# Kernel optimization log

Hardware: AMD Instinct MI355X
Metric: run time of the kernel (lower is better)

## Reference

```python
import jax, jax.numpy as jnp
import numpy as np

B, N, L = 32, 256, 50
DU, DI, DC = 32, 32, 16          # user / item / cate embed dims
D = DI + DC                       # item_feat_size = 48
N_USERS, N_ITEMS, N_CATES = 10001, 100000, 1001


def _linear_init(key, fan_in, fan_out):
    k1, k2 = jax.random.split(key)
    lim = 1.0 / np.sqrt(fan_in)
    w = jax.random.uniform(k1, (fan_in, fan_out), jnp.float32, -lim, lim)
    b = jax.random.uniform(k2, (fan_out,), jnp.float32, -lim, lim)
    return w, b


def setup_inputs() -> dict:
    key = jax.random.key(0)
    ks = jax.random.split(key, 16)

    def emb(k, n, d):
        # xavier-ish init, padding row 0 zeroed (padding_idx=0)
        t = jax.random.normal(k, (n, d), jnp.float32) * 0.02
        return t.at[0].set(0.0)

    emb_user = emb(ks[0], N_USERS, DU)
    emb_item = emb(ks[1], N_ITEMS, DI)
    emb_cate = emb(ks[2], N_CATES, DC)

    att_w1, att_b1 = _linear_init(ks[3], 4 * D, 64)   # LAU fc1 layer 1
    att_w2, att_b2 = _linear_init(ks[4], 64, 16)      # LAU fc1 layer 2
    att_w3, att_b3 = _linear_init(ks[5], 16, 1)       # LAU fc2

    TOT = DU + 2 * DI + 2 * DC                        # 128
    fc_w1, fc_b1 = _linear_init(ks[6], TOT, 200)
    fc_w2, fc_b2 = _linear_init(ks[7], 200, 80)
    fc_w3, fc_b3 = _linear_init(ks[8], 80, 1)

    user = jax.random.randint(ks[9], (B, N), 0, N_USERS)
    items = jax.random.randint(ks[10], (B, N), 0, N_ITEMS)
    items_cate = jax.random.randint(ks[11], (B, N), 0, N_CATES)
    interest_items = jax.random.randint(ks[12], (B, N, L), 0, N_ITEMS)
    interest_items_cate = jax.random.randint(ks[13], (B, N, L), 0, N_CATES)

    return dict(emb_user=emb_user, emb_item=emb_item, emb_cate=emb_cate,
                att_w1=att_w1, att_b1=att_b1, att_w2=att_w2, att_b2=att_b2,
                att_w3=att_w3, att_b3=att_b3,
                fc_w1=fc_w1, fc_b1=fc_b1, fc_w2=fc_w2, fc_b2=fc_b2,
                fc_w3=fc_w3, fc_b3=fc_b3,
                user=user, items=items, items_cate=items_cate,
                interest_items=interest_items,
                interest_items_cate=interest_items_cate)


def reference(emb_user, emb_item, emb_cate,
              att_w1, att_b1, att_w2, att_b2, att_w3, att_b3,
              fc_w1, fc_b1, fc_w2, fc_b2, fc_w3, fc_b3,
              user, items, items_cate, interest_items, interest_items_cate):
    u = emb_user[user]                                                 # [B,N,DU]
    ie = jnp.concatenate([emb_item[items], emb_cate[items_cate]], -1)  # [B,N,D]
    he = jnp.concatenate([emb_item[interest_items],
                          emb_cate[interest_items_cate]], -1)          # [B,N,L,D]

    # DIN local activation unit: cat(q, k, q-k, q*k) -> MLP -> scalar score
    q = jnp.broadcast_to(ie[:, :, None, :], he.shape)                  # [B,N,L,D]
    ai = jnp.concatenate([q, he, q - he, q * he], -1)                  # [B,N,L,4D]
    h = jax.nn.relu(ai @ att_w1 + att_b1)                              # [B,N,L,64]
    h = h @ att_w2 + att_b2                                            # [B,N,L,16]
    score = (h @ att_w3 + att_b3)[..., 0]                              # [B,N,L]

    # masked_fill(mask, 0) where mask = (interest_items == 0)
    score = jnp.where(interest_items == 0, 0.0, score)
    pooled = jnp.einsum('bnl,bnld->bnd', score, he)                    # [B,N,D]

    feat = jnp.concatenate([ie, pooled, u], -1)                        # [B,N,128]
    x = jax.nn.relu(feat @ fc_w1 + fc_b1)
    x = jax.nn.relu(x @ fc_w2 + fc_b2)
    logits = jax.nn.sigmoid((x @ fc_w3 + fc_b3)[..., 0])               # [B,N]

    logits = jnp.where(items == 0, -jnp.inf, logits)
    return jax.nn.softmax(logits, axis=-1)
```

## Files before the change

kernel.cpp:

```cpp
#include <hip/hip_runtime.h>
#include <hip/hip_bf16.h>
#include <math.h>


typedef short short8 __attribute__((ext_vector_type(8)));
typedef float f32x4 __attribute__((ext_vector_type(4)));

#define NL 50
#define BN_TOT 8192

__device__ __forceinline__ ushort f2bf(float x) {
    union { __hip_bfloat16 b; ushort u; } c;
    c.b = __float2bfloat16(x);
    return c.u;
}
__device__ __forceinline__ float bf2f(ushort h) {
    union { uint u; float f; } v; v.u = ((uint)h) << 16;
    return v.f;
}
__device__ __forceinline__ void wave_lds_fence() {
    asm volatile("s_waitcnt lgkmcnt(0)" ::: "memory");
}

#define WS_FEAT   0
#define WS_LOGITS 2097152
#define WS_W1FRAG 2129920
#define WS_W2FRAG 2183168
#define WS_WCFRAG 2226176
#define WS_WACF   2238464
#define WS_W23    2250752
#define WS_C23    2251008

__global__ __launch_bounds__(256) void k0_prep(
    const float* __restrict__ aw1, const float* __restrict__ ab1,
    const float* __restrict__ ab2,
    const float* __restrict__ aw2, const float* __restrict__ aw3,
    const float* __restrict__ ab3,
    const float* __restrict__ fw1, const float* __restrict__ fw2,
    ushort* __restrict__ W1frag, ushort* __restrict__ W2frag,
    ushort* __restrict__ WcFrag, ushort* __restrict__ WacF,
    float* __restrict__ w23, float* __restrict__ c23)
{
    const int b = blockIdx.x, t = threadIdx.x;
    if (b < 104) {
        int e = b * 256 + t;
        if (e < 26624) {
            int f = e >> 9, r = e & 511, l = r >> 3, j = r & 7;
            int nt = f >> 2, ks = f & 3;
            int k = ks * 32 + (l >> 4) * 8 + j, n = nt * 16 + (l & 15);
            float v = (n < 200) ? fw1[k * 200 + n] : 0.f;
            W1frag[e] = f2bf(v);
        }
    } else if (b < 188) {
        int e = (b - 104) * 256 + t;
        if (e < 21504) {
            int f = e >> 9, r = e & 511, l = r >> 3, j = r & 7;
            int nt = f / 7, ks = f % 7;
            int k = ks * 32 + (l >> 4) * 8 + j, n = nt * 16 + (l & 15);
            float v = (k < 200 && n < 80) ? fw2[k * 80 + n] : 0.f;
            W2frag[e] = f2bf(v);
        }
    } else if (b < 212) {
        int e = (b - 188) * 256 + t;
        int f = e >> 9, r = e & 511, l = r >> 3, j = r & 7;
        int nt = f / 3, ks = f % 3;
        int k = ks * 32 + (l >> 4) * 8 + j, n = nt * 16 + (l & 15);
        float v = (k < 48) ? (aw1[(48 + k) * 64 + n] - aw1[(96 + k) * 64 + n])
                           : aw1[(144 + (k - 48)) * 64 + n];
        WcFrag[e] = f2bf(v);
    } else if (b < 228) {
        int e = (b - 212) * 256 + t;
        int f = e >> 9, r = e & 511, l = r >> 3, j = r & 7;
        int nt = f >> 1, ks = f & 1;
        int k = ks * 32 + (l >> 4) * 8 + j, n = nt * 16 + (l & 15);
        float v = (k < 48) ? (aw1[k * 64 + n] + aw1[(96 + k) * 64 + n])
                           : ((k == 48) ? ab1[n] : 0.f);
        WacF[e] = f2bf(v);
    } else {
        if (t < 64) {
            float s = 0.f;
            #pragma unroll
            for (int jj = 0; jj < 16; ++jj) s = fmaf(aw2[t * 16 + jj], aw3[jj], s);
            w23[t] = s;
        }
        if (t == 64) {
            float c = ab3[0];
            #pragma unroll
            for (int jj = 0; jj < 16; ++jj) c = fmaf(ab2[jj], aw3[jj], c);
            c23[0] = c;
        }
    }
}

__device__ __forceinline__ short8 lds8(const ushort* hb, int row, int c) {
    return *(const short8*)&hb[row * 56 + c * 8];
}
__device__ __forceinline__ short8 scale8(const ushort* hb, const float* qv,
                                         int row, int c, int qb) {
    short8 a = lds8(hb, row, c);
    union { short8 v; ushort s[8]; } o;
    const ushort* as = (const ushort*)&a;
    #pragma unroll
    for (int j = 0; j < 8; ++j) o.s[j] = f2bf(bf2f(as[j]) * qv[qb + j]);
    return o.v;
}

__global__ __launch_bounds__(256, 4) void kA_attn(
    const float* __restrict__ emb_user,
    const float* __restrict__ emb_item,
    const float* __restrict__ emb_cate,
    const int* __restrict__ user,
    const int* __restrict__ items,
    const int* __restrict__ cates,
    const int* __restrict__ ii,
    const int* __restrict__ ic,
    const ushort* __restrict__ WcFrag,
    const ushort* __restrict__ WacF,
    const float* __restrict__ w23g,
    const float* __restrict__ c23g,
    ushort* __restrict__ feat)
{
    __shared__ __align__(16) ushort heb[4][64 * 56];
    __shared__ __align__(16) float  qf[4][48];
    __shared__ __align__(16) float  uf[4][32];
    __shared__ __align__(16) float  qcl[4][64];
    __shared__ __align__(16) float  scl[4][52];
    __shared__ int    iml[4][52];
    __shared__ int    icl[4][52];

    const int t = threadIdx.x;
    const int w = t >> 6, l = t & 63;
    const int bn = blockIdx.x * 4 + w;
    const int col = l & 15, g = l >> 4;

    ushort* hb = &heb[w][0];
    const float* qv = &qf[w][0];

    if (l < 12) {
        int it_ = items[bn], ct = cates[bn];
        float4 v = (l < 8) ? ((const float4*)emb_item)[(size_t)it_ * 8 + l]
                           : ((const float4*)emb_cate)[(size_t)ct * 4 + (l - 8)];
        *(float4*)&qf[w][l * 4] = v;
    } else if (l >= 16 && l < 24) {
        int ur = user[bn];
        *(float4*)&uf[w][(l - 16) * 4] = ((const float4*)emb_user)[(size_t)ur * 8 + (l - 16)];
    }
    if (l < NL) {
        iml[w][l] = ii[(size_t)bn * NL + l];
        icl[w][l] = ic[(size_t)bn * NL + l];
    }
    wave_lds_fence();

    #pragma unroll
    for (int e0 = 0; e0 < 300; e0 += 64) {
        int e = e0 + l;
        if (e < 300) {
            int row = e / 6, c = e - row * 6;
            int k0 = c * 8;
            const float* src = (k0 < 32)
                ? emb_item + (size_t)iml[w][row] * 32 + k0
                : emb_cate + (size_t)icl[w][row] * 16 + (k0 - 32);
            float4 f0 = *(const float4*)src;
            float4 f1 = *(const float4*)(src + 4);
            union { short8 v; ushort s[8]; } o;
            o.s[0] = f2bf(f0.x); o.s[1] = f2bf(f0.y); o.s[2] = f2bf(f0.z); o.s[3] = f2bf(f0.w);
            o.s[4] = f2bf(f1.x); o.s[5] = f2bf(f1.y); o.s[6] = f2bf(f1.z); o.s[7] = f2bf(f1.w);
            *(short8*)&hb[row * 56 + c * 8] = o.v;
        }
    }
    wave_lds_fence();

    {
        short8 afq[2];
        #pragma unroll
        for (int ks = 0; ks < 2; ++ks) {
            union { short8 v; ushort s[8]; } a;
            a.v = short8{0,0,0,0,0,0,0,0};
            if (col == 0) {
                int k0 = ks * 32 + g * 8;
                if (k0 < 48) {
                    float4 x = *(const float4*)&qf[w][k0];
                    float4 y = *(const float4*)&qf[w][k0 + 4];
                    a.s[0] = f2bf(x.x); a.s[1] = f2bf(x.y); a.s[2] = f2bf(x.z); a.s[3] = f2bf(x.w);
                    a.s[4] = f2bf(y.x); a.s[5] = f2bf(y.y); a.s[6] = f2bf(y.z); a.s[7] = f2bf(y.w);
                } else if (k0 == 48) {
                    a.s[0] = 0x3F80;
                }
            }
            afq[ks] = a.v;
        }
        f32x4 aq[4];
        #pragma unroll
        for (int nt = 0; nt < 4; ++nt) {
            aq[nt] = f32x4{0,0,0,0};
            #pragma unroll
            for (int ks = 0; ks < 2; ++ks) {
                short8 bq = *(const short8*)&WacF[((nt * 2 + ks) * 64 + l) * 8];
                aq[nt] = __builtin_amdgcn_mfma_f32_16x16x32_bf16(afq[ks], bq, aq[nt], 0, 0, 0);
            }
        }
        if (g == 0) {
            #pragma unroll
            for (int nt = 0; nt < 4; ++nt) qcl[w][nt * 16 + col] = aq[nt][0];
        }
    }

    f32x4 acc[4][4];
    #pragma unroll
    for (int m = 0; m < 4; ++m)
        #pragma unroll
        for (int n = 0; n < 4; ++n) acc[m][n] = f32x4{0,0,0,0};

    #pragma unroll
    for (int ks = 0; ks < 3; ++ks) {
        short8 af[4];
        #pragma unroll
        for (int mt = 0; mt < 4; ++mt) {
            int row = mt * 16 + col;
            if (ks == 0)       af[mt] = lds8(hb, row, g);
            else if (ks == 1)  af[mt] = (g < 2) ? lds8(hb, row, 4 + g)
                                                : scale8(hb, qv, row, g - 2, (g - 2) * 8);
            else               af[mt] = scale8(hb, qv, row, 2 + g, 16 + g * 8);
        }
        #pragma unroll
        for (int nt = 0; nt < 4; ++nt) {
            short8 bf = *(const short8*)&WcFrag[((nt * 3 + ks) * 64 + l) * 8];
            #pragma unroll
            for (int mt = 0; mt < 4; ++mt)
                acc[mt][nt] = __builtin_amdgcn_mfma_f32_16x16x32_bf16(af[mt], bf, acc[mt][nt], 0, 0, 0);
        }
    }
    wave_lds_fence();

    {
        float qcv[4], wv[4];
        #pragma unroll
        for (int nt = 0; nt < 4; ++nt) {
            qcv[nt] = qcl[w][nt * 16 + col];
            wv[nt]  = w23g[nt * 16 + col];
        }
        float c23 = c23g[0];
        #pragma unroll
        for (int mt = 0; mt < 4; ++mt) {
            #pragma unroll
            for (int i = 0; i < 4; ++i) {
                float s = fmaxf(acc[mt][0][i] + qcv[0], 0.f) * wv[0]
                        + fmaxf(acc[mt][1][i] + qcv[1], 0.f) * wv[1]
                        + fmaxf(acc[mt][2][i] + qcv[2], 0.f) * wv[2]
                        + fmaxf(acc[mt][3][i] + qcv[3], 0.f) * wv[3];
                s += __shfl_xor(s, 1, 16);
                s += __shfl_xor(s, 2, 16);
                s += __shfl_xor(s, 4, 16);
                s += __shfl_xor(s, 8, 16);
                int row = mt * 16 + g * 4 + i;
                if (col == 0 && row < NL)
                    scl[w][row] = (iml[w][row] == 0) ? 0.f : (s + c23);
            }
        }
    }
    wave_lds_fence();

    const size_t fb = (size_t)bn * 128;
    if (l < 48) {
        float p = 0.f;
        #pragma unroll
        for (int r4 = 0; r4 < 48; r4 += 4) {
            float4 sv = *(const float4*)&scl[w][r4];
            p = fmaf(sv.x, bf2f(hb[(r4 + 0) * 56 + l]), p);
            p = fmaf(sv.y, bf2f(hb[(r4 + 1) * 56 + l]), p);
            p = fmaf(sv.z, bf2f(hb[(r4 + 2) * 56 + l]), p);
            p = fmaf(sv.w, bf2f(hb[(r4 + 3) * 56 + l]), p);
        }
        float2 st = *(const float2*)&scl[w][48];
        p = fmaf(st.x, bf2f(hb[48 * 56 + l]), p);
        p = fmaf(st.y, bf2f(hb[49 * 56 + l]), p);
        feat[fb + 48 + l] = f2bf(p);
        feat[fb + l] = f2bf(qv[l]);
    }
    if (l < 32) feat[fb + 96 + l] = f2bf(uf[w][l]);
}

__global__ __launch_bounds__(64, 4) void k2_fc(
    const ushort* __restrict__ feat,
    const ushort* __restrict__ W1frag,
    const ushort* __restrict__ W2frag,
    const float* __restrict__ fb1, const float* __restrict__ fb2,
    const float* __restrict__ fw3, const float* __restrict__ fb3,
    const int* __restrict__ items,
    float* __restrict__ logits)
{
    __shared__ __align__(16) ushort x1s[16 * 256];

    const int l = threadIdx.x;
    const int r0 = blockIdx.x * 16;
    const int col = l & 15, g = l >> 4;

    short8 afr[4];
    #pragma unroll
    for (int ks = 0; ks < 4; ++ks)
        afr[ks] = *(const short8*)&feat[(size_t)(r0 + col) * 128 + ks * 32 + g * 8];

    f32x4 acc[13];
    #pragma unroll
    for (int nt = 0; nt < 13; ++nt) acc[nt] = f32x4{0,0,0,0};
    #pragma unroll
    for (int nt = 0; nt < 13; ++nt)
        #pragma unroll
        for (int ks = 0; ks < 4; ++ks) {
            short8 bf = *(const short8*)&W1frag[((nt * 4 + ks) * 64 + l) * 8];
            acc[nt] = __builtin_amdgcn_mfma_f32_16x16x32_bf16(afr[ks], bf, acc[nt], 0, 0, 0);
        }

    if (l < 32) {
        int row = l >> 1, c = 26 + (l & 1);
        *(short8*)&x1s[row * 256 + ((c ^ (row & 7)) << 3)] = short8{0,0,0,0,0,0,0,0};
    }
    #pragma unroll
    for (int nt = 0; nt < 13; ++nt) {
        int n = nt * 16 + col;
        float bias = (n < 200) ? fb1[n] : 0.f;
        #pragma unroll
        for (int i = 0; i < 4; ++i) {
            int row = g * 4 + i;
            float v = fmaxf(acc[nt][i] + bias, 0.f);
            int sw = (n >> 3) ^ (row & 7);
            x1s[row * 256 + sw * 8 + (n & 7)] = f2bf(v);
        }
    }
    wave_lds_fence();

    f32x4 acc2[6];
    #pragma unroll
    for (int nt = 0; nt < 6; ++nt) acc2[nt] = f32x4{0,0,0,0};
    #pragma unroll
    for (int ks = 0; ks < 7; ++ks) {
        int chunk = ks * 4 + g;
        short8 a = *(const short8*)&x1s[col * 256 + ((chunk ^ (col & 7)) << 3)];
        #pragma unroll
        for (int nt = 0; nt < 6; ++nt) {
            short8 bf = *(const short8*)&W2frag[((nt * 7 + ks) * 64 + l) * 8];
            acc2[nt] = __builtin_amdgcn_mfma_f32_16x16x32_bf16(a, bf, acc2[nt], 0, 0, 0);
        }
    }

    {
        float s[4] = {0.f, 0.f, 0.f, 0.f};
        #pragma unroll
        for (int nt = 0; nt < 5; ++nt) {
            int n = nt * 16 + col;
            float b2v = fb2[n], w3v = fw3[n];
            #pragma unroll
            for (int i = 0; i < 4; ++i)
                s[i] = fmaf(fmaxf(acc2[nt][i] + b2v, 0.f), w3v, s[i]);
        }
        #pragma unroll
        for (int i = 0; i < 4; ++i) {
            s[i] += __shfl_xor(s[i], 1, 16);
            s[i] += __shfl_xor(s[i], 2, 16);
            s[i] += __shfl_xor(s[i], 4, 16);
            s[i] += __shfl_xor(s[i], 8, 16);
        }
        if (col == 0) {
            float b3 = fb3[0];
            #pragma unroll
            for (int i = 0; i < 4; ++i) {
                int row = r0 + g * 4 + i;
                float lg = (items[row] == 0) ? -INFINITY
                                             : 1.f / (1.f + __expf(-(s[i] + b3)));
                logits[row] = lg;
            }
        }
    }
}

__global__ __launch_bounds__(256) void k3_softmax(
    const float* __restrict__ logits, float* __restrict__ out)
{
    const int b = blockIdx.x, t = threadIdx.x;
    __shared__ float red[4];
    float v = logits[b * 256 + t];
    float m = v;
    #pragma unroll
    for (int off = 32; off; off >>= 1) m = fmaxf(m, __shfl_xor(m, off, 64));
    if ((t & 63) == 0) red[t >> 6] = m;
    __syncthreads();
    float mx = fmaxf(fmaxf(red[0], red[1]), fmaxf(red[2], red[3]));
    float e = __expf(v - mx);
    float s = e;
    #pragma unroll
    for (int off = 32; off; off >>= 1) s += __shfl_xor(s, off, 64);
    __syncthreads();
    if ((t & 63) == 0) red[t >> 6] = s;
    __syncthreads();
    float tot = red[0] + red[1] + red[2] + red[3];
    out[b * 256 + t] = e / tot;
}

extern "C" void kernel_launch(void* const* d_in, const int* in_sizes, int n_in,
                              void* d_out, int out_size, void* d_ws, size_t ws_size,
                              hipStream_t stream)
{
    const float* emb_user = (const float*)d_in[0];
    const float* emb_item = (const float*)d_in[1];
    const float* emb_cate = (const float*)d_in[2];
    const float* aw1 = (const float*)d_in[3];
    const float* ab1 = (const float*)d_in[4];
    const float* aw2 = (const float*)d_in[5];
    const float* ab2 = (const float*)d_in[6];
    const float* aw3 = (const float*)d_in[7];
    const float* ab3 = (const float*)d_in[8];
    const float* fw1 = (const float*)d_in[9];
    const float* fb1 = (const float*)d_in[10];
    const float* fw2 = (const float*)d_in[11];
    const float* fb2 = (const float*)d_in[12];
    const float* fw3 = (const float*)d_in[13];
    const float* fb3 = (const float*)d_in[14];
    const int* user  = (const int*)d_in[15];
    const int* items = (const int*)d_in[16];
    const int* cates = (const int*)d_in[17];
    const int* ii    = (const int*)d_in[18];
    const int* ic    = (const int*)d_in[19];

    char* ws = (char*)d_ws;
    ushort* feat   = (ushort*)(ws + WS_FEAT);
    float*  logits = (float*) (ws + WS_LOGITS);
    ushort* W1frag = (ushort*)(ws + WS_W1FRAG);
    ushort* W2frag = (ushort*)(ws + WS_W2FRAG);
    ushort* WcFrag = (ushort*)(ws + WS_WCFRAG);
    ushort* WacF   = (ushort*)(ws + WS_WACF);
    float*  w23    = (float*) (ws + WS_W23);
    float*  c23    = (float*) (ws + WS_C23);

    k0_prep<<<229, 256, 0, stream>>>(aw1, ab1, ab2, aw2, aw3, ab3, fw1, fw2,
                                     W1frag, W2frag, WcFrag, WacF, w23, c23);
    kA_attn<<<BN_TOT / 4, 256, 0, stream>>>(emb_user, emb_item, emb_cate,
                                            user, items, cates, ii, ic,
                                            WcFrag, WacF, w23, c23, feat);
    k2_fc<<<BN_TOT / 16, 64, 0, stream>>>(feat, W1frag, W2frag,
                                          fb1, fb2, fw3, fb3, items, logits);
    k3_softmax<<<32, 256, 0, stream>>>(logits, (float*)d_out);
}
```

Measured before the change: 142.1 us.

## Fuse FC MLP into attention kernel and pre-convert embedding tables to bf16

Adds a pass that converts the item, category and user embedding tables to bf16 in the workspace, so the attention kernel gathers half the bytes per row and skips per-element conversion. The FC MLP that used to be a separate kernel is now fused into the attention kernel: the 4 waves share a 16-row feature tile in LDS (padded with zero rows), split the FC1/FC2 N-tiles between them and reduce the final dot product across waves. This removes the feat round-trip through global memory and one launch, and raises the occupancy hint to 5. The cost is converting the whole 100k-row item table on every call, plus block-level syncs and MFMA work wasted on 12 of the 16 padded rows.

Result: slower. 159.5 us (+12.2%).

```diff
diff --git a/kernel.cpp b/kernel.cpp
--- a/kernel.cpp
+++ b/kernel.cpp
@@ -22,7 +22,6 @@
     asm volatile("s_waitcnt lgkmcnt(0)" ::: "memory");
 }
 
-#define WS_FEAT   0
 #define WS_LOGITS 2097152
 #define WS_W1FRAG 2129920
 #define WS_W2FRAG 2183168
@@ -30,6 +29,25 @@
 #define WS_WACF   2238464
 #define WS_W23    2250752
 #define WS_C23    2251008
+#define WS_EBI    2251264
+#define WS_EBC    8651264
+#define WS_EBU    8683296
+
+__global__ __launch_bounds__(256) void k0_tables(
+    const float* __restrict__ ei, const float* __restrict__ ec,
+    const float* __restrict__ eu,
+    ushort* __restrict__ obi, ushort* __restrict__ obc, ushort* __restrict__ obu)
+{
+    int e = blockIdx.x * 256 + threadIdx.x;
+    if (e >= 884012) return;
+    const float4* src; ushort4* dst; int i;
+    if (e < 800000)      { src = (const float4*)ei; dst = (ushort4*)obi; i = e; }
+    else if (e < 804004) { src = (const float4*)ec; dst = (ushort4*)obc; i = e - 800000; }
+    else                 { src = (const float4*)eu; dst = (ushort4*)obu; i = e - 804004; }
+    float4 v = src[i];
+    ushort4 o; o.x = f2bf(v.x); o.y = f2bf(v.y); o.z = f2bf(v.z); o.w = f2bf(v.w);
+    dst[i] = o;
+}
 
 __global__ __launch_bounds__(256) void k0_prep(
     const float* __restrict__ aw1, const float* __restrict__ ab1,
@@ -105,10 +123,9 @@
     return o.v;
 }
 
-__global__ __launch_bounds__(256, 4) void kA_attn(
-    const float* __restrict__ emb_user,
-    const float* __restrict__ emb_item,
-    const float* __restrict__ emb_cate,
+__global__ __launch_bounds__(256, 5) void kA_attn(
+    const ushort* __restrict__ ebi, const ushort* __restrict__ ebc,
+    const ushort* __restrict__ ebu,
     const int* __restrict__ user,
     const int* __restrict__ items,
     const int* __restrict__ cates,
@@ -118,36 +135,51 @@
     const ushort* __restrict__ WacF,
     const float* __restrict__ w23g,
     const float* __restrict__ c23g,
-    ushort* __restrict__ feat)
+    const ushort* __restrict__ W1frag,
+    const ushort* __restrict__ W2frag,
+    const float* __restrict__ fb1, const float* __restrict__ fb2,
+    const float* __restrict__ fw3, const float* __restrict__ fb3,
+    float* __restrict__ logits)
 {
-    __shared__ __align__(16) ushort heb[4][64 * 56];
-    __shared__ __align__(16) float  qf[4][48];
-    __shared__ __align__(16) float  uf[4][32];
-    __shared__ __align__(16) float  qcl[4][64];
-    __shared__ __align__(16) float  scl[4][52];
-    __shared__ int    iml[4][52];
-    __shared__ int    icl[4][52];
+    __shared__ __align__(16) char LDSBUF[31232];
+    ushort* hebA  = (ushort*)LDSBUF;
+    float*  qfA   = (float*) (LDSBUF + 22400);
+    float*  qclA  = (float*) (LDSBUF + 23168);
+    float*  sclA  = (float*) (LDSBUF + 24192);
+    int*    imlA  = (int*)   (LDSBUF + 25024);
+    int*    iclA  = (int*)   (LDSBUF + 25856);
+    ushort* fL    = (ushort*)(LDSBUF + 26688);
+    float*  part  = (float*) (LDSBUF + 31040);
+    ushort* x1s   = (ushort*)LDSBUF;
 
     const int t = threadIdx.x;
     const int w = t >> 6, l = t & 63;
     const int bn = blockIdx.x * 4 + w;
     const int col = l & 15, g = l >> 4;
 
-    ushort* hb = &heb[w][0];
-    const float* qv = &qf[w][0];
-
-    if (l < 12) {
-        int it_ = items[bn], ct = cates[bn];
-        float4 v = (l < 8) ? ((const float4*)emb_item)[(size_t)it_ * 8 + l]
-                           : ((const float4*)emb_cate)[(size_t)ct * 4 + (l - 8)];
-        *(float4*)&qf[w][l * 4] = v;
-    } else if (l >= 16 && l < 24) {
-        int ur = user[bn];
-        *(float4*)&uf[w][(l - 16) * 4] = ((const float4*)emb_user)[(size_t)ur * 8 + (l - 16)];
+    ushort* hb = hebA + w * 2800;
+    float*  qv = qfA + w * 48;
+
+    const int it_ = items[bn], ct = cates[bn], ur = user[bn];
+
+    if (l < 6) {
+        short8 v = (l < 4) ? *(const short8*)&ebi[(size_t)it_ * 32 + l * 8]
+                           : *(const short8*)&ebc[(size_t)ct * 16 + (l - 4) * 8];
+        const ushort* vs = (const ushort*)&v;
+        #pragma unroll
+        for (int j = 0; j < 8; ++j) qv[l * 8 + j] = bf2f(vs[j]);
+        *(short8*)&fL[w * 136 + l * 8] = v;
+    } else if (l >= 8 && l < 12) {
+        short8 v = *(const short8*)&ebu[(size_t)ur * 32 + (l - 8) * 8];
+        *(short8*)&fL[w * 136 + 96 + (l - 8) * 8] = v;
     }
     if (l < NL) {
-        iml[w][l] = ii[(size_t)bn * NL + l];
-        icl[w][l] = ic[(size_t)bn * NL + l];
+        imlA[w * 52 + l] = ii[(size_t)bn * NL + l];
+        iclA[w * 52 + l] = ic[(size_t)bn * NL + l];
+    }
+    for (int e = t; e < 204; e += 256) {
+        int row = 4 + e / 17, ch = e % 17;
+        *(short8*)&fL[row * 136 + ch * 8] = short8{0,0,0,0,0,0,0,0};
     }
     wave_lds_fence();
 
@@ -156,16 +188,10 @@
         int e = e0 + l;
         if (e < 300) {
             int row = e / 6, c = e - row * 6;
-            int k0 = c * 8;
-            const float* src = (k0 < 32)
-                ? emb_item + (size_t)iml[w][row] * 32 + k0
-                : emb_cate + (size_t)icl[w][row] * 16 + (k0 - 32);
-            float4 f0 = *(const float4*)src;
-            float4 f1 = *(const float4*)(src + 4);
-            union { short8 v; ushort s[8]; } o;
-            o.s[0] = f2bf(f0.x); o.s[1] = f2bf(f0.y); o.s[2] = f2bf(f0.z); o.s[3] = f2bf(f0.w);
-            o.s[4] = f2bf(f1.x); o.s[5] = f2bf(f1.y); o.s[6] = f2bf(f1.z); o.s[7] = f2bf(f1.w);
-            *(short8*)&hb[row * 56 + c * 8] = o.v;
+            short8 v = (c < 4)
+                ? *(const short8*)&ebi[(size_t)imlA[w * 52 + row] * 32 + c * 8]
+                : *(const short8*)&ebc[(size_t)iclA[w * 52 + row] * 16 + (c - 4) * 8];
+            *(short8*)&hb[row * 56 + c * 8] = v;
         }
     }
     wave_lds_fence();
@@ -179,8 +205,8 @@
             if (col == 0) {
                 int k0 = ks * 32 + g * 8;
                 if (k0 < 48) {
-                    float4 x = *(const float4*)&qf[w][k0];
-                    float4 y = *(const float4*)&qf[w][k0 + 4];
+                    float4 x = *(const float4*)&qv[k0];
+                    float4 y = *(const float4*)&qv[k0 + 4];
                     a.s[0] = f2bf(x.x); a.s[1] = f2bf(x.y); a.s[2] = f2bf(x.z); a.s[3] = f2bf(x.w);
                     a.s[4] = f2bf(y.x); a.s[5] = f2bf(y.y); a.s[6] = f2bf(y.z); a.s[7] = f2bf(y.w);
                 } else if (k0 == 48) {
@@ -201,7 +227,7 @@
         }
         if (g == 0) {
             #pragma unroll
-            for (int nt = 0; nt < 4; ++nt) qcl[w][nt * 16 + col] = aq[nt][0];
+            for (int nt = 0; nt < 4; ++nt) qclA[w * 64 + nt * 16 + col] = aq[nt][0];
         }
     }
 
@@ -217,10 +243,14 @@
         #pragma unroll
         for (int mt = 0; mt < 4; ++mt) {
             int row = mt * 16 + col;
-            if (ks == 0)       af[mt] = lds8(hb, row, g);
-            else if (ks == 1)  af[mt] = (g < 2) ? lds8(hb, row, 4 + g)
-                                                : scale8(hb, qv, row, g - 2, (g - 2) * 8);
-            else               af[mt] = scale8(hb, qv, row, 2 + g, 16 + g * 8);
+            short8 v = short8{0,0,0,0,0,0,0,0};
+            if (row < 50) {
+                if (ks == 0)      v = lds8(hb, row, g);
+                else if (ks == 1) v = (g < 2) ? lds8(hb, row, 4 + g)
+                                              : scale8(hb, qv, row, g - 2, (g - 2) * 8);
+                else              v = scale8(hb, qv, row, 2 + g, 16 + g * 8);
+            }
+            af[mt] = v;
         }
         #pragma unroll
         for (int nt = 0; nt < 4; ++nt) {
@@ -236,7 +266,7 @@
         float qcv[4], wv[4];
         #pragma unroll
         for (int nt = 0; nt < 4; ++nt) {
-            qcv[nt] = qcl[w][nt * 16 + col];
+            qcv[nt] = qclA[w * 64 + nt * 16 + col];
             wv[nt]  = w23g[nt * 16 + col];
         }
         float c23 = c23g[0];
@@ -254,122 +284,116 @@
                 s += __shfl_xor(s, 8, 16);
                 int row = mt * 16 + g * 4 + i;
                 if (col == 0 && row < NL)
-                    scl[w][row] = (iml[w][row] == 0) ? 0.f : (s + c23);
+                    sclA[w * 52 + row] = (imlA[w * 52 + row] == 0) ? 0.f : (s + c23);
             }
         }
     }
     wave_lds_fence();
 
-    const size_t fb = (size_t)bn * 128;
     if (l < 48) {
         float p = 0.f;
         #pragma unroll
         for (int r4 = 0; r4 < 48; r4 += 4) {
-            float4 sv = *(const float4*)&scl[w][r4];
+            float4 sv = *(const float4*)&sclA[w * 52 + r4];
             p = fmaf(sv.x, bf2f(hb[(r4 + 0) * 56 + l]), p);
             p = fmaf(sv.y, bf2f(hb[(r4 + 1) * 56 + l]), p);
             p = fmaf(sv.z, bf2f(hb[(r4 + 2) * 56 + l]), p);
             p = fmaf(sv.w, bf2f(hb[(r4 + 3) * 56 + l]), p);
         }
-        float2 st = *(const float2*)&scl[w][48];
+        float2 st = *(const float2*)&sclA[w * 52 + 48];
         p = fmaf(st.x, bf2f(hb[48 * 56 + l]), p);
         p = fmaf(st.y, bf2f(hb[49 * 56 + l]), p);
-        feat[fb + 48 + l] = f2bf(p);
-        feat[fb + l] = f2bf(qv[l]);
-    }
-    if (l < 32) feat[fb + 96 + l] = f2bf(uf[w][l]);
-}
-
-__global__ __launch_bounds__(64, 4) void k2_fc(
-    const ushort* __restrict__ feat,
-    const ushort* __restrict__ W1frag,
-    const ushort* __restrict__ W2frag,
-    const float* __restrict__ fb1, const float* __restrict__ fb2,
-    const float* __restrict__ fw3, const float* __restrict__ fb3,
-    const int* __restrict__ items,
-    float* __restrict__ logits)
-{
-    __shared__ __align__(16) ushort x1s[16 * 256];
-
-    const int l = threadIdx.x;
-    const int r0 = blockIdx.x * 16;
-    const int col = l & 15, g = l >> 4;
+        fL[w * 136 + 48 + l] = f2bf(p);
+    }
+    __syncthreads();
 
     short8 afr[4];
     #pragma unroll
     for (int ks = 0; ks < 4; ++ks)
-        afr[ks] = *(const short8*)&feat[(size_t)(r0 + col) * 128 + ks * 32 + g * 8];
-
-    f32x4 acc[13];
-    #pragma unroll
-    for (int nt = 0; nt < 13; ++nt) acc[nt] = f32x4{0,0,0,0};
-    #pragma unroll
-    for (int nt = 0; nt < 13; ++nt)
-        #pragma unroll
-        for (int ks = 0; ks < 4; ++ks) {
-            short8 bf = *(const short8*)&W1frag[((nt * 4 + ks) * 64 + l) * 8];
-            acc[nt] = __builtin_amdgcn_mfma_f32_16x16x32_bf16(afr[ks], bf, acc[nt], 0, 0, 0);
-        }
-
-    if (l < 32) {
+        afr[ks] = *(const short8*)&fL[col * 136 + ks * 32 + g * 8];
+
+    const int nt_lo1  = (w == 0) ? 0 : 3 * w + 1;
+    const int nt_cnt1 = (w == 0) ? 4 : 3;
+    f32x4 acc1[4];
+    #pragma unroll
+    for (int q_ = 0; q_ < 4; ++q_) acc1[q_] = f32x4{0,0,0,0};
+    #pragma unroll
+    for (int q_ = 0; q_ < 4; ++q_) {
+        if (q_ < nt_cnt1) {
+            int nt = nt_lo1 + q_;
+            #pragma unroll
+            for (int ks = 0; ks < 4; ++ks) {
+                short8 bf = *(const short8*)&W1frag[((nt * 4 + ks) * 64 + l) * 8];
+                acc1[q_] = __builtin_amdgcn_mfma_f32_16x16x32_bf16(afr[ks], bf, acc1[q_], 0, 0, 0);
+            }
+        }
+    }
+    if (w == 3 && l < 32) {
         int row = l >> 1, c = 26 + (l & 1);
         *(short8*)&x1s[row * 256 + ((c ^ (row & 7)) << 3)] = short8{0,0,0,0,0,0,0,0};
     }
     #pragma unroll
-    for (int nt = 0; nt < 13; ++nt) {
-        int n = nt * 16 + col;
-        float bias = (n < 200) ? fb1[n] : 0.f;
-        #pragma unroll
-        for (int i = 0; i < 4; ++i) {
-            int row = g * 4 + i;
-            float v = fmaxf(acc[nt][i] + bias, 0.f);
-            int sw = (n >> 3) ^ (row & 7);
-            x1s[row * 256 + sw * 8 + (n & 7)] = f2bf(v);
-        }
-    }
-    wave_lds_fence();
-
-    f32x4 acc2[6];
-    #pragma unroll
-    for (int nt = 0; nt < 6; ++nt) acc2[nt] = f32x4{0,0,0,0};
-    #pragma unroll
-    for (int ks = 0; ks < 7; ++ks) {
-        int chunk = ks * 4 + g;
-        short8 a = *(const short8*)&x1s[col * 256 + ((chunk ^ (col & 7)) << 3)];
-        #pragma unroll
-        for (int nt = 0; nt < 6; ++nt) {
-            short8 bf = *(const short8*)&W2frag[((nt * 7 + ks) * 64 + l) * 8];
-            acc2[nt] = __builtin_amdgcn_mfma_f32_16x16x32_bf16(a, bf, acc2[nt], 0, 0, 0);
-        }
-    }
-
-    {
-        float s[4] = {0.f, 0.f, 0.f, 0.f};
-        #pragma unroll
-        for (int nt = 0; nt < 5; ++nt) {
+    for (int q_ = 0; q_ < 4; ++q_) {
+        if (q_ < nt_cnt1) {
+            int nt = nt_lo1 + q_;
             int n = nt * 16 + col;
-            float b2v = fb2[n], w3v = fw3[n];
-            #pragma unroll
-            for (int i = 0; i < 4; ++i)
-                s[i] = fmaf(fmaxf(acc2[nt][i] + b2v, 0.f), w3v, s[i]);
-        }
-        #pragma unroll
-        for (int i = 0; i < 4; ++i) {
-            s[i] += __shfl_xor(s[i], 1, 16);
-            s[i] += __shfl_xor(s[i], 2, 16);
-            s[i] += __shfl_xor(s[i], 4, 16);
-            s[i] += __shfl_xor(s[i], 8, 16);
-        }
-        if (col == 0) {
-            float b3 = fb3[0];
+            float bias = (n < 200) ? fb1[n] : 0.f;
             #pragma unroll
             for (int i = 0; i < 4; ++i) {
-                int row = r0 + g * 4 + i;
-                float lg = (items[row] == 0) ? -INFINITY
-                                             : 1.f / (1.f + __expf(-(s[i] + b3)));
-                logits[row] = lg;
-            }
-        }
+                int row = g * 4 + i;
+                float vv = fmaxf(acc1[q_][i] + bias, 0.f);
+                int sw = (n >> 3) ^ (row & 7);
+                x1s[row * 256 + sw * 8 + (n & 7)] = f2bf(vv);
+            }
+        }
+    }
+    __syncthreads();
+
+    const int nt_cnt2 = (w < 2) ? 2 : (w == 2 ? 1 : 0);
+    float s3[4] = {0.f, 0.f, 0.f, 0.f};
+    if (nt_cnt2 > 0) {
+        short8 a2f[7];
+        #pragma unroll
+        for (int ks = 0; ks < 7; ++ks) {
+            int chunk = ks * 4 + g;
+            a2f[ks] = *(const short8*)&x1s[col * 256 + ((chunk ^ (col & 7)) << 3)];
+        }
+        #pragma unroll
+        for (int q_ = 0; q_ < 2; ++q_) {
+            if (q_ < nt_cnt2) {
+                int nt = w * 2 + q_;
+                f32x4 a2 = f32x4{0,0,0,0};
+                #pragma unroll
+                for (int ks = 0; ks < 7; ++ks) {
+                    short8 bf = *(const short8*)&W2frag[((nt * 7 + ks) * 64 + l) * 8];
+                    a2 = __builtin_amdgcn_mfma_f32_16x16x32_bf16(a2f[ks], bf, a2, 0, 0, 0);
+                }
+                int n = nt * 16 + col;
+                float b2v = fb2[n], w3v = fw3[n];
+                #pragma unroll
+                for (int i = 0; i < 4; ++i)
+                    s3[i] = fmaf(fmaxf(a2[i] + b2v, 0.f), w3v, s3[i]);
+            }
+        }
+    }
+    #pragma unroll
+    for (int i = 0; i < 4; ++i) {
+        s3[i] += __shfl_xor(s3[i], 1, 16);
+        s3[i] += __shfl_xor(s3[i], 2, 16);
+        s3[i] += __shfl_xor(s3[i], 4, 16);
+        s3[i] += __shfl_xor(s3[i], 8, 16);
+    }
+    if (w < 3 && col == 0 && g == 0) {
+        #pragma unroll
+        for (int i = 0; i < 4; ++i) part[w * 4 + i] = s3[i];
+    }
+    __syncthreads();
+
+    if (t < 4) {
+        float s = part[t] + part[4 + t] + part[8 + t] + fb3[0];
+        int row = blockIdx.x * 4 + t;
+        float lg = (items[row] == 0) ? -INFINITY : 1.f / (1.f + __expf(-s));
+        logits[row] = lg;
     }
 }
 
@@ -422,7 +446,6 @@
     const int* ic    = (const int*)d_in[19];
 
     char* ws = (char*)d_ws;
-    ushort* feat   = (ushort*)(ws + WS_FEAT);
     float*  logits = (float*) (ws + WS_LOGITS);
     ushort* W1frag = (ushort*)(ws + WS_W1FRAG);
     ushort* W2frag = (ushort*)(ws + WS_W2FRAG);
@@ -430,13 +453,17 @@
     ushort* WacF   = (ushort*)(ws + WS_WACF);
     float*  w23    = (float*) (ws + WS_W23);
     float*  c23    = (float*) (ws + WS_C23);
-
+    ushort* ebi    = (ushort*)(ws + WS_EBI);
+    ushort* ebc    = (ushort*)(ws + WS_EBC);
+    ushort* ebu    = (ushort*)(ws + WS_EBU);
+
+    k0_tables<<<3454, 256, 0, stream>>>(emb_item, emb_cate, emb_user, ebi, ebc, ebu);
     k0_prep<<<229, 256, 0, stream>>>(aw1, ab1, ab2, aw2, aw3, ab3, fw1, fw2,
                                      W1frag, W2frag, WcFrag, WacF, w23, c23);
-    kA_attn<<<BN_TOT / 4, 256, 0, stream>>>(emb_user, emb_item, emb_cate,
+    kA_attn<<<BN_TOT / 4, 256, 0, stream>>>(ebi, ebc, ebu,
                                             user, items, cates, ii, ic,
-                                            WcFrag, WacF, w23, c23, feat);
-    k2_fc<<<BN_TOT / 16, 64, 0, stream>>>(feat, W1frag, W2frag,
-                                          fb1, fb2, fw3, fb3, items, logits);
+                                            WcFrag, WacF, w23, c23,
+                                            W1frag, W2frag, fb1, fb2, fw3, fb3,
+                                            logits);
     k3_softmax<<<32, 256, 0, stream>>>(logits, (float*)d_out);
 }
```

## Shrink attention kernel LDS footprint and raise occupancy target

Applied to the files above, without the earlier changes.

The attention kernel packs its shared arrays into one tightly sized buffer that stores only the 50 used history rows per wave, drops the separate user and category-index LDS arrays, and raises the launch-bounds occupancy hint from 4 to 6 blocks. Gather indices are read straight from global memory into registers, so the index-load-then-fence step before the embedding gather is removed. The query and user embeddings are converted and written to the feature output early, using vector stores instead of per-element ones. MFMA rows past 50 are zero-filled instead of reading unused LDS. The tighter occupancy bound may cause register pressure or spills.

Result: slower. 178.8 us (+25.8%).

```diff
diff --git a/kernel.cpp b/kernel.cpp
--- a/kernel.cpp
+++ b/kernel.cpp
@@ -104,8 +104,14 @@
     for (int j = 0; j < 8; ++j) o.s[j] = f2bf(bf2f(as[j]) * qv[qb + j]);
     return o.v;
 }
-
-__global__ __launch_bounds__(256, 4) void kA_attn(
+__device__ __forceinline__ short8 cvt8(float4 f0, float4 f1) {
+    union { short8 v; ushort s[8]; } o;
+    o.s[0] = f2bf(f0.x); o.s[1] = f2bf(f0.y); o.s[2] = f2bf(f0.z); o.s[3] = f2bf(f0.w);
+    o.s[4] = f2bf(f1.x); o.s[5] = f2bf(f1.y); o.s[6] = f2bf(f1.z); o.s[7] = f2bf(f1.w);
+    return o.v;
+}
+
+__global__ __launch_bounds__(256, 6) void kA_attn(
     const float* __restrict__ emb_user,
     const float* __restrict__ emb_item,
     const float* __restrict__ emb_cate,
@@ -120,52 +126,62 @@
     const float* __restrict__ c23g,
     ushort* __restrict__ feat)
 {
-    __shared__ __align__(16) ushort heb[4][64 * 56];
-    __shared__ __align__(16) float  qf[4][48];
-    __shared__ __align__(16) float  uf[4][32];
-    __shared__ __align__(16) float  qcl[4][64];
-    __shared__ __align__(16) float  scl[4][52];
-    __shared__ int    iml[4][52];
-    __shared__ int    icl[4][52];
+    __shared__ __align__(16) char LDSBUF[25856];
+    ushort* hebA  = (ushort*)LDSBUF;
+    float*  qfA   = (float*) (LDSBUF + 22400);
+    float*  qclA  = (float*) (LDSBUF + 23168);
+    float*  sclA  = (float*) (LDSBUF + 24192);
+    int*    imlA  = (int*)   (LDSBUF + 25024);
 
     const int t = threadIdx.x;
     const int w = t >> 6, l = t & 63;
     const int bn = blockIdx.x * 4 + w;
     const int col = l & 15, g = l >> 4;
 
-    ushort* hb = &heb[w][0];
-    const float* qv = &qf[w][0];
-
-    if (l < 12) {
-        int it_ = items[bn], ct = cates[bn];
-        float4 v = (l < 8) ? ((const float4*)emb_item)[(size_t)it_ * 8 + l]
-                           : ((const float4*)emb_cate)[(size_t)ct * 4 + (l - 8)];
-        *(float4*)&qf[w][l * 4] = v;
-    } else if (l >= 16 && l < 24) {
-        int ur = user[bn];
-        *(float4*)&uf[w][(l - 16) * 4] = ((const float4*)emb_user)[(size_t)ur * 8 + (l - 16)];
-    }
-    if (l < NL) {
-        iml[w][l] = ii[(size_t)bn * NL + l];
-        icl[w][l] = ic[(size_t)bn * NL + l];
-    }
-    wave_lds_fence();
-
-    #pragma unroll
-    for (int e0 = 0; e0 < 300; e0 += 64) {
-        int e = e0 + l;
-        if (e < 300) {
-            int row = e / 6, c = e - row * 6;
-            int k0 = c * 8;
-            const float* src = (k0 < 32)
-                ? emb_item + (size_t)iml[w][row] * 32 + k0
-                : emb_cate + (size_t)icl[w][row] * 16 + (k0 - 32);
-            float4 f0 = *(const float4*)src;
-            float4 f1 = *(const float4*)(src + 4);
-            union { short8 v; ushort s[8]; } o;
-            o.s[0] = f2bf(f0.x); o.s[1] = f2bf(f0.y); o.s[2] = f2bf(f0.z); o.s[3] = f2bf(f0.w);
-            o.s[4] = f2bf(f1.x); o.s[5] = f2bf(f1.y); o.s[6] = f2bf(f1.z); o.s[7] = f2bf(f1.w);
-            *(short8*)&hb[row * 56 + c * 8] = o.v;
+    ushort* hb = hebA + w * 2800;
+    float*  qv = qfA + w * 48;
+
+    const int it_ = items[bn], ct = cates[bn], ur = user[bn];
+    const size_t fb = (size_t)bn * 128;
+
+    if (l < 6) {
+        const float* p = (l < 4) ? emb_item + (size_t)it_ * 32 + l * 8
+                                 : emb_cate + (size_t)ct * 16 + (l - 4) * 8;
+        float4 f0 = *(const float4*)p, f1 = *(const float4*)(p + 4);
+        *(float4*)&qv[l * 8]     = f0;
+        *(float4*)&qv[l * 8 + 4] = f1;
+        *(short8*)&feat[fb + l * 8] = cvt8(f0, f1);
+    } else if (l >= 8 && l < 12) {
+        const float* p = emb_user + (size_t)ur * 32 + (l - 8) * 8;
+        float4 f0 = *(const float4*)p, f1 = *(const float4*)(p + 4);
+        *(short8*)&feat[fb + 96 + (l - 8) * 8] = cvt8(f0, f1);
+    }
+    if (l < NL) imlA[w * 52 + l] = ii[(size_t)bn * NL + l];
+
+    {
+        int idxs[5];
+        #pragma unroll
+        for (int j = 0; j < 5; ++j) {
+            int e = 64 * j + l;
+            if (e < 300) {
+                int row = e / 6, c = e - row * 6;
+                idxs[j] = (c < 4) ? ii[(size_t)bn * NL + row]
+                                  : ic[(size_t)bn * NL + row];
+            }
+        }
+        #pragma unroll
+        for (int j = 0; j < 5; ++j) {
+            int e = 64 * j + l;
+            if (e < 300) {
+                int row = e / 6, c = e - row * 6;
+                int k0 = c * 8;
+                const float* src = (k0 < 32)
+                    ? emb_item + (size_t)idxs[j] * 32 + k0
+                    : emb_cate + (size_t)idxs[j] * 16 + (k0 - 32);
+                float4 f0 = *(const float4*)src;
+                float4 f1 = *(const float4*)(src + 4);
+                *(short8*)&hb[row * 56 + c * 8] = cvt8(f0, f1);
+            }
         }
     }
     wave_lds_fence();
@@ -179,10 +195,9 @@
             if (col == 0) {
                 int k0 = ks * 32 + g * 8;
                 if (k0 < 48) {
-                    float4 x = *(const float4*)&qf[w][k0];
-                    float4 y = *(const float4*)&qf[w][k0 + 4];
-                    a.s[0] = f2bf(x.x); a.s[1] = f2bf(x.y); a.s[2] = f2bf(x.z); a.s[3] = f2bf(x.w);
-                    a.s[4] = f2bf(y.x); a.s[5] = f2bf(y.y); a.s[6] = f2bf(y.z); a.s[7] = f2bf(y.w);
+                    float4 x = *(const float4*)&qv[k0];
+                    float4 y = *(const float4*)&qv[k0 + 4];
+                    a.v = cvt8(x, y);
                 } else if (k0 == 48) {
                     a.s[0] = 0x3F80;
                 }
@@ -201,7 +216,7 @@
         }
         if (g == 0) {
             #pragma unroll
-            for (int nt = 0; nt < 4; ++nt) qcl[w][nt * 16 + col] = aq[nt][0];
+            for (int nt = 0; nt < 4; ++nt) qclA[w * 64 + nt * 16 + col] = aq[nt][0];
         }
     }
 
@@ -217,10 +232,14 @@
         #pragma unroll
         for (int mt = 0; mt < 4; ++mt) {
             int row = mt * 16 + col;
-            if (ks == 0)       af[mt] = lds8(hb, row, g);
-            else if (ks == 1)  af[mt] = (g < 2) ? lds8(hb, row, 4 + g)
-                                                : scale8(hb, qv, row, g - 2, (g - 2) * 8);
-            else               af[mt] = scale8(hb, qv, row, 2 + g, 16 + g * 8);
+            short8 v = short8{0,0,0,0,0,0,0,0};
+            if (row < 50) {
+                if (ks == 0)      v = lds8(hb, row, g);
+                else if (ks == 1) v = (g < 2) ? lds8(hb, row, 4 + g)
+                                              : scale8(hb, qv, row, g - 2, (g - 2) * 8);
+                else              v = scale8(hb, qv, row, 2 + g, 16 + g * 8);
+            }
+            af[mt] = v;
         }
         #pragma unroll
         for (int nt = 0; nt < 4; ++nt) {
@@ -236,7 +255,7 @@
         float qcv[4], wv[4];
         #pragma unroll
         for (int nt = 0; nt < 4; ++nt) {
-            qcv[nt] = qcl[w][nt * 16 + col];
+            qcv[nt] = qclA[w * 64 + nt * 16 + col];
             wv[nt]  = w23g[nt * 16 + col];
         }
         float c23 = c23g[0];
@@ -254,30 +273,27 @@
                 s += __shfl_xor(s, 8, 16);
                 int row = mt * 16 + g * 4 + i;
                 if (col == 0 && row < NL)
-                    scl[w][row] = (iml[w][row] == 0) ? 0.f : (s + c23);
+                    sclA[w * 52 + row] = (imlA[w * 52 + row] == 0) ? 0.f : (s + c23);
             }
         }
     }
     wave_lds_fence();
 
-    const size_t fb = (size_t)bn * 128;
     if (l < 48) {
         float p = 0.f;
         #pragma unroll
         for (int r4 = 0; r4 < 48; r4 += 4) {
-            float4 sv = *(const float4*)&scl[w][r4];
+            float4 sv = *(const float4*)&sclA[w * 52 + r4];
             p = fmaf(sv.x, bf2f(hb[(r4 + 0) * 56 + l]), p);
             p = fmaf(sv.y, bf2f(hb[(r4 + 1) * 56 + l]), p);
             p = fmaf(sv.z, bf2f(hb[(r4 + 2) * 56 + l]), p);
             p = fmaf(sv.w, bf2f(hb[(r4 + 3) * 56 + l]), p);
         }
-        float2 st = *(const float2*)&scl[w][48];
+        float2 st = *(const float2*)&sclA[w * 52 + 48];
         p = fmaf(st.x, bf2f(hb[48 * 56 + l]), p);
         p = fmaf(st.y, bf2f(hb[49 * 56 + l]), p);
         feat[fb + 48 + l] = f2bf(p);
-        feat[fb + l] = f2bf(qv[l]);
-    }
-    if (l < 32) feat[fb + 96 + l] = f2bf(uf[w][l]);
+    }
 }
 
 __global__ __launch_bounds__(64, 4) void k2_fc(
```
